# Kernel tuning notes

Hardware: AMD Instinct MI355X
Metric: run time of the kernel (lower is better)

## Reference

```python
import jax, jax.numpy as jnp
import numpy as np

B, S, D, H = 2, 2048, 1024, 16
HD = D // H  # head_dim = 64


def setup_inputs() -> dict:
    key = jax.random.key(0)
    ks = jax.random.split(key, 12)
    sc = 0.02
    return {
        "query": jax.random.normal(ks[0], (B, S, D), jnp.float32),
        "key": jax.random.normal(ks[1], (B, S, D), jnp.float32),
        "value": jax.random.normal(ks[2], (B, S, D), jnp.float32),
        "key_padding_mask": jax.random.randint(ks[3], (B, S), 0, 2).astype(bool),
        "attn_mask": jax.random.randint(ks[4], (B, S), 0, 2).astype(bool),
        "is_casual": 0,
        "Wq": jax.random.normal(ks[5], (D, D), jnp.float32) * sc,
        "bq": jnp.zeros((D,), jnp.float32),
        "Wk": jax.random.normal(ks[6], (D, D), jnp.float32) * sc,
        "bk": jnp.zeros((D,), jnp.float32),
        "Wv": jax.random.normal(ks[7], (D, D), jnp.float32) * sc,
        "bv": jnp.zeros((D,), jnp.float32),
        "Wo": jax.random.normal(ks[8], (D, D), jnp.float32) * sc,
        "bo": jnp.zeros((D,), jnp.float32),
    }


def reference(query, key, value, key_padding_mask, attn_mask, is_casual,
              Wq, bq, Wk, bk, Wv, bv, Wo, bo):
    b, s, _ = query.shape
    # projections (torch Linear: x @ W.T + b)
    Q = query @ Wq.T + bq
    K = key @ Wk.T + bk
    V = value @ Wv.T + bv
    # [B, H, S, HD]
    Q = Q.reshape(b, s, H, HD).transpose(0, 2, 1, 3)
    K = K.reshape(b, s, H, HD).transpose(0, 2, 1, 3)
    V = V.reshape(b, s, H, HD).transpose(0, 2, 1, 3)
    scores = jnp.einsum("bhqd,bhkd->bhqk", Q, K) / jnp.sqrt(jnp.float32(HD))
    neg_inf = jnp.float32(-jnp.inf)
    # both masks broadcast over the key axis: [B,1,1,S]
    scores = jnp.where(key_padding_mask[:, None, None, :], neg_inf, scores)
    scores = jnp.where(attn_mask[:, None, None, :], neg_inf, scores)
    # is_casual only applies in training mode; eval reference: no causal mask, no dropout
    attn = jax.nn.softmax(scores, axis=-1)
    x = jnp.einsum("bhqk,bhkd->bhqd", attn, V)
    x = x.transpose(0, 2, 1, 3).reshape(b, s, D)
    return x @ Wo.T + bo
```

## Files before the change

### kernel.cpp

```cpp
#include <hip/hip_runtime.h>


typedef __attribute__((ext_vector_type(8))) short short8;
typedef __attribute__((ext_vector_type(4))) float f32x4;
typedef __attribute__((ext_vector_type(4))) int int32x4;

#define MFMA16(a, b, c) __builtin_amdgcn_mfma_f32_16x16x32_bf16(a, b, c, 0, 0, 0)

#define GLL16(gp, lp) __builtin_amdgcn_global_load_lds( \
    (const __attribute__((address_space(1))) void*)(gp), \
    (__attribute__((address_space(3))) void*)(lp), 16, 0, 0)

static __device__ __forceinline__ unsigned short f2bf(float x) {
    unsigned int u = __float_as_uint(x);
    u = (u + 0x7fffu + ((u >> 16) & 1u)) >> 16;
    return (unsigned short)u;
}

__global__ __launch_bounds__(256)
void scan_kernel(const int* __restrict__ kpm, const int* __restrict__ am,
                 int* __restrict__ map, int* __restrict__ cnt)
{
    const int b = blockIdx.x, tid = threadIdx.x;
    const int lane = tid & 63, wave = tid >> 6;
    __shared__ int wtot[4];
    int flag[8]; int c = 0;
    const int base = b * 2048 + tid * 8;
#pragma unroll
    for (int e = 0; e < 8; ++e) {
        flag[e] = (kpm[base + e] | am[base + e]) ? 0 : 1;
        c += flag[e];
    }
    int pre = c;
#pragma unroll
    for (int off = 1; off < 64; off <<= 1) {
        const int t = __shfl_up(pre, off, 64);
        if (lane >= off) pre += t;
    }
    if (lane == 63) wtot[wave] = pre;
    __syncthreads();
    int woff = 0;
#pragma unroll
    for (int w = 0; w < 4; ++w) if (w < wave) woff += wtot[w];
    const int total = wtot[0] + wtot[1] + wtot[2] + wtot[3];
    if (tid == 0) cnt[b] = total;
    int off = b * 2048 + woff + (pre - c);
    const int s0 = tid * 8;
#pragma unroll
    for (int e = 0; e < 8; ++e)
        if (flag[e]) map[off++] = s0 + e;
    __syncthreads();
    const int first = (total > 0) ? map[b * 2048] : 0;
    for (int j = total + tid; j < 2048; j += 256)
        map[b * 2048 + j] = first;
}

__global__ __launch_bounds__(256)
void conv_many(const float* __restrict__ s0, unsigned short* __restrict__ d0, int n0,
               const float* __restrict__ s1, unsigned short* __restrict__ d1, int n1,
               const float* __restrict__ s2, unsigned short* __restrict__ d2, int n2,
               const float* __restrict__ s3, unsigned short* __restrict__ d3, int n3,
               const float* __restrict__ s4, unsigned short* __restrict__ d4, int n4,
               const float* __restrict__ s5, unsigned short* __restrict__ d5, int n5)
{
    const int y = blockIdx.y;
    const float* s; unsigned short* d; int n;
    if (y == 0)      { s = s0; d = d0; n = n0; }
    else if (y == 1) { s = s1; d = d1; n = n1; }
    else if (y == 2) { s = s2; d = d2; n = n2; }
    else if (y == 3) { s = s3; d = d3; n = n3; }
    else if (y == 4) { s = s4; d = d4; n = n4; }
    else             { s = s5; d = d5; n = n5; }
    const int i = (blockIdx.x * 256 + threadIdx.x) * 8;
    if (i >= n) return;
    const float4 a = *(const float4*)(s + i);
    const float4 b = *(const float4*)(s + i + 4);
    ushort4 lo, hi;
    lo.x = f2bf(a.x); lo.y = f2bf(a.y); lo.z = f2bf(a.z); lo.w = f2bf(a.w);
    hi.x = f2bf(b.x); hi.y = f2bf(b.y); hi.z = f2bf(b.z); hi.w = f2bf(b.w);
    *(ushort4*)(d + i) = lo;
    *(ushort4*)(d + i + 4) = hi;
}

template<int OUT_MODE, bool GATHER>
static __device__ __forceinline__
void gemm_core(int sub, const unsigned short* __restrict__ A, const unsigned short* __restrict__ Wb,
               const float* __restrict__ bias, float alpha, void* __restrict__ outp,
               unsigned short* sm, const int* __restrict__ map, const int* __restrict__ cnt)
{
    constexpr int N = 1024, K = 1024;
    const int xcd = sub & 7, loc = sub >> 3;
    const int m0 = (xcd * 4 + (loc >> 4)) * 128;
    const int n0 = (loc & 15) * 64;

    const int tid = threadIdx.x, lane = tid & 63, wave = tid >> 6;
    const int lr = lane & 15, quad = lane >> 4;
    const int wm = (wave >> 1) * 64, wn = (wave & 1) * 32;
    const int lr3 = lane >> 3;
    const int qcs = (lane & 7) ^ lr3;

    const int bb = m0 >> 11;
    int arow[4];
    if constexpr (GATHER) {
        const int cntb = cnt[bb];
        int cnt64 = (cntb + 63) & ~63;
        if (cnt64 < 64) cnt64 = 64;
        if ((m0 & 2047) >= cnt64) return;
#pragma unroll
        for (int n = 0; n < 4; n++) {
            const int row = (wave * 4 + n) * 8 + lr3;
            arow[n] = bb * 2048 + map[bb * 2048 + (m0 & 2047) + row];
        }
    } else {
#pragma unroll
        for (int n = 0; n < 4; n++)
            arow[n] = m0 + (wave * 4 + n) * 8 + lr3;
    }

    f32x4 acc[4][2];
#pragma unroll
    for (int mt = 0; mt < 4; mt++)
#pragma unroll
        for (int nt = 0; nt < 2; nt++) acc[mt][nt] = (f32x4){0.f, 0.f, 0.f, 0.f};

    auto stg = [&](int t) {
        unsigned short* Asb = sm + (t & 1) * 12288;
        unsigned short* Bsb = Asb + 8192;
        const int k0 = t * 64;
#pragma unroll
        for (int n = 0; n < 4; n++) {
            const int W = wave * 4 + n;
            GLL16(A + (size_t)arow[n] * K + k0 + qcs * 8, Asb + W * 512);
        }
#pragma unroll
        for (int n = 0; n < 2; n++) {
            const int W = wave * 2 + n;
            const int row = W * 8 + lr3;
            GLL16(Wb + (size_t)(n0 + row) * K + k0 + qcs * 8, Bsb + W * 512);
        }
    };

    stg(0);

    for (int it = 0; it < 16; ++it) {
        __syncthreads();
        if (it + 1 < 16) stg(it + 1);
        const unsigned short* Asc = sm + (it & 1) * 12288;
        const unsigned short* Bsc = Asc + 8192;
#pragma unroll
        for (int kc = 0; kc < 2; kc++) {
            short8 af[4], bfr[2];
#pragma unroll
            for (int mt = 0; mt < 4; mt++) {
                const int r = wm + mt * 16 + lr;
                af[mt] = *(const short8*)&Asc[(r * 8 + ((kc * 4 + quad) ^ (r & 7))) * 8];
            }
#pragma unroll
            for (int nt = 0; nt < 2; nt++) {
                const int r = wn + nt * 16 + lr;
                bfr[nt] = *(const short8*)&Bsc[(r * 8 + ((kc * 4 + quad) ^ (r & 7))) * 8];
            }
#pragma unroll
            for (int mt = 0; mt < 4; mt++)
#pragma unroll
                for (int nt = 0; nt < 2; nt++)
                    acc[mt][nt] = MFMA16(af[mt], bfr[nt], acc[mt][nt]);
        }
    }

    if constexpr (OUT_MODE == 2) {
        constexpr int LDT = 136;
        __syncthreads();
        unsigned short* Ts = sm;
#pragma unroll
        for (int mt = 0; mt < 4; mt++)
#pragma unroll
            for (int nt = 0; nt < 2; nt++) {
                const int dd = wn + nt * 16 + lr;
                const int ss = wm + mt * 16 + quad * 4;
                const int j = n0 + dd;
                ushort4 tv;
                tv.x = f2bf(alpha * (acc[mt][nt][0] + bias[j]));
                tv.y = f2bf(alpha * (acc[mt][nt][1] + bias[j]));
                tv.z = f2bf(alpha * (acc[mt][nt][2] + bias[j]));
                tv.w = f2bf(alpha * (acc[mt][nt][3] + bias[j]));
                *(ushort4*)&Ts[dd * LDT + ss] = tv;
            }
        __syncthreads();
        const int b = m0 >> 11, hh = (n0 >> 6) & 15, sbase = m0 & 2047;
        const int row = tid >> 2, c4 = (tid & 3) * 32;
        unsigned short* dst = (unsigned short*)outp
            + (((size_t)(b * 16 + hh) * 64) + row) * 2048 + sbase + c4;
#pragma unroll
        for (int t = 0; t < 4; ++t)
            *(short8*)&dst[t * 8] = *(const short8*)&Ts[row * LDT + c4 + t * 8];
        return;
    }

#pragma unroll
    for (int mt = 0; mt < 4; mt++)
#pragma unroll
        for (int nt = 0; nt < 2; nt++)
#pragma unroll
            for (int r = 0; r < 4; r++) {
                const int i = m0 + wm + mt * 16 + quad * 4 + r;
                const int j = n0 + wn + nt * 16 + lr;
                const float val = alpha * (acc[mt][nt][r] + bias[j]);
                if constexpr (OUT_MODE == 0) {
                    ((float*)outp)[(size_t)i * N + j] = val;
                } else {
                    const int b = i >> 11, s = i & 2047, hh = j >> 6, dd = j & 63;
                    ((unsigned short*)outp)[(((size_t)(b * 16 + hh) * 2048) + s) * 64 + dd] = f2bf(val);
                }
            }
}

__global__ __launch_bounds__(256)
void gemm_qv(const unsigned short* __restrict__ qb, const unsigned short* __restrict__ wqb,
             const float* __restrict__ bq, float alpha_q, void* __restrict__ Qh,
             const unsigned short* __restrict__ vb, const unsigned short* __restrict__ wvb,
             const float* __restrict__ bv, void* __restrict__ Vt,
             const int* __restrict__ map, const int* __restrict__ cnt)
{
    __shared__ unsigned short sm[24576];
    const int id = blockIdx.x, sub = id & 511;
    if (id < 512) gemm_core<1, false>(sub, qb, wqb, bq, alpha_q, Qh, sm, nullptr, nullptr);
    else          gemm_core<2, true >(sub, vb, wvb, bv, 1.0f,   Vt, sm, map, cnt);
}

template<int OUT_MODE, bool GATHER>
__global__ __launch_bounds__(256)
void gemm_one(const unsigned short* __restrict__ A, const unsigned short* __restrict__ Wb,
              const float* __restrict__ bias, float alpha, void* __restrict__ outp,
              const int* __restrict__ map, const int* __restrict__ cnt)
{
    __shared__ unsigned short sm[24576];
    gemm_core<OUT_MODE, GATHER>(blockIdx.x, A, Wb, bias, alpha, outp, sm, map, cnt);
}

__global__ __launch_bounds__(256)
void attn_kernel(const unsigned short* __restrict__ Qh, const unsigned short* __restrict__ Kh,
                 const unsigned short* __restrict__ Vt, const int* __restrict__ kpm,
                 const int* __restrict__ am, unsigned short* __restrict__ ctx)
{
    const int qb = blockIdx.x, bh = blockIdx.y, b = bh >> 4, h = bh & 15;
    const int q0 = qb * 64;
    const int tid = threadIdx.x, lane = tid & 63, wave = tid >> 6;
    const int lr = lane & 15, quad = lane >> 4;

    __shared__ unsigned short Ks[2][64 * 64];
    __shared__ unsigned short Vs[2][64 * 64];
    __shared__ int wred[4];

    {
        int c = 0;
        const int mb = b * 2048 + tid * 8;
#pragma unroll
        for (int e = 0; e < 8; ++e)
            c += (kpm[mb + e] | am[mb + e]) ? 0 : 1;
#pragma unroll
        for (int off = 32; off > 0; off >>= 1)
            c += __shfl_xor(c, off, 64);
        if (lane == 0) wred[wave] = c;
    }
    __syncthreads();
    const int cntb = wred[0] + wred[1] + wred[2] + wred[3];
    const int nits = (cntb > 0) ? ((cntb + 63) >> 6) : 1;

    const unsigned short* Kbh = Kh + (size_t)bh * 2048 * 64;
    const unsigned short* Vbh = Vt + (size_t)bh * 64 * 2048;

    const int lr3 = lane >> 3;
    const int qcs = (lane & 7) ^ lr3;

    auto stage = [&](int buf, int k0) {
#pragma unroll
        for (int n = 0; n < 2; ++n) {
            const int W = wave + n * 4;
            const int r = W * 8 + lr3;
            GLL16(Kbh + (size_t)(k0 + r) * 64 + qcs * 8, &Ks[buf][W * 512]);
            GLL16(Vbh + (size_t)r * 2048 + k0 + qcs * 8, &Vs[buf][W * 512]);
        }
    };

    const unsigned short* Qbase = Qh + ((size_t)bh * 2048 + q0 + wave * 16 + lr) * 64 + quad * 8;
    const short8 qf0 = *(const short8*)Qbase;
    const short8 qf1 = *(const short8*)(Qbase + 32);

    short8 onesA;
#pragma unroll
    for (int j = 0; j < 8; j++) onesA[j] = (short)0x3F80;

    f32x4 o[4];
    f32x4 lacc = (f32x4){0.f, 0.f, 0.f, 0.f};
#pragma unroll
    for (int nt = 0; nt < 4; nt++) o[nt] = (f32x4){0.f, 0.f, 0.f, 0.f};

    const int srcA = (quad & 1) * 32 + lr;
    const int srcB = srcA + 16;

    int koff[2][2][2], voff[2][4];
#pragma unroll
    for (int s32 = 0; s32 < 2; ++s32) {
#pragma unroll
        for (int tt = 0; tt < 2; ++tt) {
            const int kk = (s32 * 2 + tt) * 16 + lr;
            koff[s32][tt][0] = (kk * 8 + (quad ^ (kk & 7))) * 8;
            koff[s32][tt][1] = (kk * 8 + ((quad + 4) ^ (kk & 7))) * 8;
        }
#pragma unroll
        for (int nt = 0; nt < 4; ++nt) {
            const int d = nt * 16 + lr;
            const int qc = s32 * 4 + quad;
            voff[s32][nt] = (d * 8 + (qc ^ (d & 7))) * 8;
        }
    }

    auto tile = [&](const unsigned short* __restrict__ Kb,
                    const unsigned short* __restrict__ Vb, int k0) {
#pragma unroll
        for (int s32 = 0; s32 < 2; ++s32) {
            unsigned int pk[2][2];
#pragma unroll
            for (int tt = 0; tt < 2; ++tt) {
                const short8 kf0 = *(const short8*)&Kb[koff[s32][tt][0]];
                const short8 kf1 = *(const short8*)&Kb[koff[s32][tt][1]];
                f32x4 z;
                if (k0 + 64 <= cntb) {
                    z = (f32x4){0.f, 0.f, 0.f, 0.f};
                } else {
                    const int jb = k0 + (s32 * 2 + tt) * 16 + quad * 4;
#pragma unroll
                    for (int r = 0; r < 4; ++r)
                        z[r] = (jb + r < cntb) ? 0.f : -1e5f;
                }
                z = MFMA16(kf0, qf0, z);
                z = MFMA16(kf1, qf1, z);
                const float p0 = __builtin_amdgcn_exp2f(z[0]);
                const float p1 = __builtin_amdgcn_exp2f(z[1]);
                const float p2 = __builtin_amdgcn_exp2f(z[2]);
                const float p3 = __builtin_amdgcn_exp2f(z[3]);
                pk[tt][0] = ((unsigned)f2bf(p1) << 16) | f2bf(p0);
                pk[tt][1] = ((unsigned)f2bf(p3) << 16) | f2bf(p2);
            }
            const int a0 = __shfl((int)pk[0][0], srcA, 64);
            const int a1 = __shfl((int)pk[0][1], srcA, 64);
            const int a2 = __shfl((int)pk[0][0], srcB, 64);
            const int a3 = __shfl((int)pk[0][1], srcB, 64);
            const int c0 = __shfl((int)pk[1][0], srcA, 64);
            const int c1 = __shfl((int)pk[1][1], srcA, 64);
            const int c2 = __shfl((int)pk[1][0], srcB, 64);
            const int c3 = __shfl((int)pk[1][1], srcB, 64);
            const bool hi = quad >= 2;
            union { int32x4 i; short8 s; } u;
            u.i = (int32x4){hi ? c0 : a0, hi ? c1 : a1, hi ? c2 : a2, hi ? c3 : a3};
            const short8 pb = u.s;

            lacc = MFMA16(onesA, pb, lacc);
#pragma unroll
            for (int nt = 0; nt < 4; ++nt) {
                const short8 vf = *(const short8*)&Vb[voff[s32][nt]];
                o[nt] = MFMA16(vf, pb, o[nt]);
            }
        }
    };

    stage(0, 0);

    for (int it = 0; it < nits; ++it) {
        __syncthreads();
        if (it + 1 < nits) stage((it + 1) & 1, (it + 1) * 64);
        if (it & 1) tile(Ks[1], Vs[1], it * 64);
        else        tile(Ks[0], Vs[0], it * 64);
    }

    const float linv = 1.f / lacc[0];
    const int srow = q0 + wave * 16 + lr;
#pragma unroll
    for (int nt = 0; nt < 4; ++nt) {
        ushort4 pk4;
        pk4.x = f2bf(o[nt][0] * linv);
        pk4.y = f2bf(o[nt][1] * linv);
        pk4.z = f2bf(o[nt][2] * linv);
        pk4.w = f2bf(o[nt][3] * linv);
        *(ushort4*)&ctx[((size_t)(b * 2048 + srow)) * 1024 + h * 64 + nt * 16 + quad * 4] = pk4;
    }
}

extern "C" void kernel_launch(void* const* d_in, const int* in_sizes, int n_in,
                              void* d_out, int out_size, void* d_ws, size_t ws_size,
                              hipStream_t stream)
{
    const float* query = (const float*)d_in[0];
    const float* key_  = (const float*)d_in[1];
    const float* value = (const float*)d_in[2];
    const int* kpm     = (const int*)d_in[3];
    const int* am      = (const int*)d_in[4];
    const float* Wq = (const float*)d_in[6];
    const float* bq = (const float*)d_in[7];
    const float* Wk = (const float*)d_in[8];
    const float* bk = (const float*)d_in[9];
    const float* Wv = (const float*)d_in[10];
    const float* bv = (const float*)d_in[11];
    const float* Wo = (const float*)d_in[12];
    const float* bo = (const float*)d_in[13];

    unsigned short* ws16 = (unsigned short*)d_ws;
    unsigned short* Qh  = ws16;
    unsigned short* kbn = ws16 + (1u << 22);
    unsigned short* wob = ws16 + (1u << 22);
    unsigned short* Vt  = ws16 + (2u << 22);
    unsigned short* ctx = ws16 + 3 * (1u << 22);
    unsigned short* wqb = ctx;
    unsigned short* wvb = ctx + (1u << 20);
    unsigned short* wkb = ctx + (2u << 20);
    int* map = (int*)(ctx + (3u << 20));
    int* cnt = map + 4096;

    unsigned short* ob  = (unsigned short*)d_out;
    unsigned short* qb  = ob;
    unsigned short* vb  = ob + (1u << 22);
    unsigned short* Khd = ob;

    const dim3 blk(256);
    const float alpha_q = 0.125f * 1.4426950408889634f;

    scan_kernel<<<2, blk, 0, stream>>>(kpm, am, map, cnt);
    conv_many<<<dim3(2048, 6), blk, 0, stream>>>(
        query, qb,  1 << 22,
        value, vb,  1 << 22,
        key_,  kbn, 1 << 22,
        Wq,    wqb, 1 << 20,
        Wv,    wvb, 1 << 20,
        Wk,    wkb, 1 << 20);
    gemm_qv<<<1024, blk, 0, stream>>>(qb, wqb, bq, alpha_q, (void*)Qh, vb, wvb, bv, (void*)Vt,
                                      map, cnt);
    gemm_one<1, true><<<512, blk, 0, stream>>>(kbn, wkb, bk, 1.0f, (void*)Khd, map, cnt);
    conv_many<<<dim3(512, 1), blk, 0, stream>>>(
        Wo, wob, 1 << 20,
        nullptr, nullptr, 0, nullptr, nullptr, 0,
        nullptr, nullptr, 0, nullptr, nullptr, 0, nullptr, nullptr, 0);
    attn_kernel<<<dim3(32, 32), blk, 0, stream>>>(Qh, Khd, Vt, kpm, am, ctx);
    gemm_one<0, false><<<512, blk, 0, stream>>>(ctx, wob, bo, 1.0f, d_out, nullptr, nullptr);
}
```

Before: 207.1 us.

## Double query rows per attention block and fold mask scan into conversion launch

The attention kernel now has each block handle 128 query rows instead of 64. Each wave holds two sets of Q fragments and accumulators, so every K/V tile staged in LDS is used for twice as many queries and total K/V traffic is halved. This raises register pressure and halves the attention grid to 512 blocks, which may lower occupancy. The separate mask scan kernel is also merged into the input conversion launch as an extra grid row, and the Wo conversion uses a simpler dedicated kernel, removing one launch.

Result: no change. 207.4 us (+0.1%).

```diff
diff --git a/kernel.cpp b/kernel.cpp
--- a/kernel.cpp
+++ b/kernel.cpp
@@ -18,52 +18,52 @@
 }
 
 __global__ __launch_bounds__(256)
-void scan_kernel(const int* __restrict__ kpm, const int* __restrict__ am,
-                 int* __restrict__ map, int* __restrict__ cnt)
-{
-    const int b = blockIdx.x, tid = threadIdx.x;
-    const int lane = tid & 63, wave = tid >> 6;
-    __shared__ int wtot[4];
-    int flag[8]; int c = 0;
-    const int base = b * 2048 + tid * 8;
-#pragma unroll
-    for (int e = 0; e < 8; ++e) {
-        flag[e] = (kpm[base + e] | am[base + e]) ? 0 : 1;
-        c += flag[e];
-    }
-    int pre = c;
-#pragma unroll
-    for (int off = 1; off < 64; off <<= 1) {
-        const int t = __shfl_up(pre, off, 64);
-        if (lane >= off) pre += t;
-    }
-    if (lane == 63) wtot[wave] = pre;
-    __syncthreads();
-    int woff = 0;
-#pragma unroll
-    for (int w = 0; w < 4; ++w) if (w < wave) woff += wtot[w];
-    const int total = wtot[0] + wtot[1] + wtot[2] + wtot[3];
-    if (tid == 0) cnt[b] = total;
-    int off = b * 2048 + woff + (pre - c);
-    const int s0 = tid * 8;
-#pragma unroll
-    for (int e = 0; e < 8; ++e)
-        if (flag[e]) map[off++] = s0 + e;
-    __syncthreads();
-    const int first = (total > 0) ? map[b * 2048] : 0;
-    for (int j = total + tid; j < 2048; j += 256)
-        map[b * 2048 + j] = first;
-}
-
-__global__ __launch_bounds__(256)
-void conv_many(const float* __restrict__ s0, unsigned short* __restrict__ d0, int n0,
+void conv_scan(const float* __restrict__ s0, unsigned short* __restrict__ d0, int n0,
                const float* __restrict__ s1, unsigned short* __restrict__ d1, int n1,
                const float* __restrict__ s2, unsigned short* __restrict__ d2, int n2,
                const float* __restrict__ s3, unsigned short* __restrict__ d3, int n3,
                const float* __restrict__ s4, unsigned short* __restrict__ d4, int n4,
-               const float* __restrict__ s5, unsigned short* __restrict__ d5, int n5)
+               const float* __restrict__ s5, unsigned short* __restrict__ d5, int n5,
+               const int* __restrict__ kpm, const int* __restrict__ am,
+               int* __restrict__ map, int* __restrict__ cnt)
 {
     const int y = blockIdx.y;
+    if (y == 6) {
+        if (blockIdx.x >= 2) return;
+        const int b = blockIdx.x, tid = threadIdx.x;
+        const int lane = tid & 63, wave = tid >> 6;
+        __shared__ int wtot[4];
+        int flag[8]; int c = 0;
+        const int base = b * 2048 + tid * 8;
+#pragma unroll
+        for (int e = 0; e < 8; ++e) {
+            flag[e] = (kpm[base + e] | am[base + e]) ? 0 : 1;
+            c += flag[e];
+        }
+        int pre = c;
+#pragma unroll
+        for (int off = 1; off < 64; off <<= 1) {
+            const int t = __shfl_up(pre, off, 64);
+            if (lane >= off) pre += t;
+        }
+        if (lane == 63) wtot[wave] = pre;
+        __syncthreads();
+        int woff = 0;
+#pragma unroll
+        for (int w = 0; w < 4; ++w) if (w < wave) woff += wtot[w];
+        const int total = wtot[0] + wtot[1] + wtot[2] + wtot[3];
+        if (tid == 0) cnt[b] = total;
+        int off = b * 2048 + woff + (pre - c);
+        const int s0i = tid * 8;
+#pragma unroll
+        for (int e = 0; e < 8; ++e)
+            if (flag[e]) map[off++] = s0i + e;
+        __syncthreads();
+        const int first = (total > 0) ? map[b * 2048] : 0;
+        for (int j = total + tid; j < 2048; j += 256)
+            map[b * 2048 + j] = first;
+        return;
+    }
     const float* s; unsigned short* d; int n;
     if (y == 0)      { s = s0; d = d0; n = n0; }
     else if (y == 1) { s = s1; d = d1; n = n1; }
@@ -82,6 +82,20 @@
     *(ushort4*)(d + i + 4) = hi;
 }
 
+__global__ __launch_bounds__(256)
+void conv_one(const float* __restrict__ s, unsigned short* __restrict__ d, int n)
+{
+    const int i = (blockIdx.x * 256 + threadIdx.x) * 8;
+    if (i >= n) return;
+    const float4 a = *(const float4*)(s + i);
+    const float4 b = *(const float4*)(s + i + 4);
+    ushort4 lo, hi;
+    lo.x = f2bf(a.x); lo.y = f2bf(a.y); lo.z = f2bf(a.z); lo.w = f2bf(a.w);
+    hi.x = f2bf(b.x); hi.y = f2bf(b.y); hi.z = f2bf(b.z); hi.w = f2bf(b.w);
+    *(ushort4*)(d + i) = lo;
+    *(ushort4*)(d + i + 4) = hi;
+}
+
 template<int OUT_MODE, bool GATHER>
 static __device__ __forceinline__
 void gemm_core(int sub, const unsigned short* __restrict__ A, const unsigned short* __restrict__ Wb,
@@ -244,7 +258,7 @@
                  const int* __restrict__ am, unsigned short* __restrict__ ctx)
 {
     const int qb = blockIdx.x, bh = blockIdx.y, b = bh >> 4, h = bh & 15;
-    const int q0 = qb * 64;
+    const int q0 = qb * 128;
     const int tid = threadIdx.x, lane = tid & 63, wave = tid >> 6;
     const int lr = lane & 15, quad = lane >> 4;
 
@@ -284,17 +298,23 @@
     };
 
     const unsigned short* Qbase = Qh + ((size_t)bh * 2048 + q0 + wave * 16 + lr) * 64 + quad * 8;
-    const short8 qf0 = *(const short8*)Qbase;
-    const short8 qf1 = *(const short8*)(Qbase + 32);
+    const short8 qf0a = *(const short8*)Qbase;
+    const short8 qf1a = *(const short8*)(Qbase + 32);
+    const short8 qf0b = *(const short8*)(Qbase + 64 * 64);
+    const short8 qf1b = *(const short8*)(Qbase + 64 * 64 + 32);
 
     short8 onesA;
 #pragma unroll
     for (int j = 0; j < 8; j++) onesA[j] = (short)0x3F80;
 
-    f32x4 o[4];
-    f32x4 lacc = (f32x4){0.f, 0.f, 0.f, 0.f};
-#pragma unroll
-    for (int nt = 0; nt < 4; nt++) o[nt] = (f32x4){0.f, 0.f, 0.f, 0.f};
+    f32x4 oA[4], oB[4];
+    f32x4 laccA = (f32x4){0.f, 0.f, 0.f, 0.f};
+    f32x4 laccB = (f32x4){0.f, 0.f, 0.f, 0.f};
+#pragma unroll
+    for (int nt = 0; nt < 4; nt++) {
+        oA[nt] = (f32x4){0.f, 0.f, 0.f, 0.f};
+        oB[nt] = (f32x4){0.f, 0.f, 0.f, 0.f};
+    }
 
     const int srcA = (quad & 1) * 32 + lr;
     const int srcB = srcA + 16;
@@ -320,47 +340,70 @@
                     const unsigned short* __restrict__ Vb, int k0) {
 #pragma unroll
         for (int s32 = 0; s32 < 2; ++s32) {
-            unsigned int pk[2][2];
+            unsigned int pkA[2][2], pkB[2][2];
 #pragma unroll
             for (int tt = 0; tt < 2; ++tt) {
                 const short8 kf0 = *(const short8*)&Kb[koff[s32][tt][0]];
                 const short8 kf1 = *(const short8*)&Kb[koff[s32][tt][1]];
-                f32x4 z;
+                f32x4 zm;
                 if (k0 + 64 <= cntb) {
-                    z = (f32x4){0.f, 0.f, 0.f, 0.f};
+                    zm = (f32x4){0.f, 0.f, 0.f, 0.f};
                 } else {
                     const int jb = k0 + (s32 * 2 + tt) * 16 + quad * 4;
 #pragma unroll
                     for (int r = 0; r < 4; ++r)
-                        z[r] = (jb + r < cntb) ? 0.f : -1e5f;
+                        zm[r] = (jb + r < cntb) ? 0.f : -1e5f;
                 }
-                z = MFMA16(kf0, qf0, z);
-                z = MFMA16(kf1, qf1, z);
-                const float p0 = __builtin_amdgcn_exp2f(z[0]);
-                const float p1 = __builtin_amdgcn_exp2f(z[1]);
-                const float p2 = __builtin_amdgcn_exp2f(z[2]);
-                const float p3 = __builtin_amdgcn_exp2f(z[3]);
-                pk[tt][0] = ((unsigned)f2bf(p1) << 16) | f2bf(p0);
-                pk[tt][1] = ((unsigned)f2bf(p3) << 16) | f2bf(p2);
-            }
-            const int a0 = __shfl((int)pk[0][0], srcA, 64);
-            const int a1 = __shfl((int)pk[0][1], srcA, 64);
-            const int a2 = __shfl((int)pk[0][0], srcB, 64);
-            const int a3 = __shfl((int)pk[0][1], srcB, 64);
-            const int c0 = __shfl((int)pk[1][0], srcA, 64);
-            const int c1 = __shfl((int)pk[1][1], srcA, 64);
-            const int c2 = __shfl((int)pk[1][0], srcB, 64);
-            const int c3 = __shfl((int)pk[1][1], srcB, 64);
+                f32x4 zA = zm, zB = zm;
+                zA = MFMA16(kf0, qf0a, zA);
+                zA = MFMA16(kf1, qf1a, zA);
+                zB = MFMA16(kf0, qf0b, zB);
+                zB = MFMA16(kf1, qf1b, zB);
+                pkA[tt][0] = ((unsigned)f2bf(__builtin_amdgcn_exp2f(zA[1])) << 16)
+                           | f2bf(__builtin_amdgcn_exp2f(zA[0]));
+                pkA[tt][1] = ((unsigned)f2bf(__builtin_amdgcn_exp2f(zA[3])) << 16)
+                           | f2bf(__builtin_amdgcn_exp2f(zA[2]));
+                pkB[tt][0] = ((unsigned)f2bf(__builtin_amdgcn_exp2f(zB[1])) << 16)
+                           | f2bf(__builtin_amdgcn_exp2f(zB[0]));
+                pkB[tt][1] = ((unsigned)f2bf(__builtin_amdgcn_exp2f(zB[3])) << 16)
+                           | f2bf(__builtin_amdgcn_exp2f(zB[2]));
+            }
             const bool hi = quad >= 2;
-            union { int32x4 i; short8 s; } u;
-            u.i = (int32x4){hi ? c0 : a0, hi ? c1 : a1, hi ? c2 : a2, hi ? c3 : a3};
-            const short8 pb = u.s;
-
-            lacc = MFMA16(onesA, pb, lacc);
+            short8 pbA, pbB;
+            {
+                const int a0 = __shfl((int)pkA[0][0], srcA, 64);
+                const int a1 = __shfl((int)pkA[0][1], srcA, 64);
+                const int a2 = __shfl((int)pkA[0][0], srcB, 64);
+                const int a3 = __shfl((int)pkA[0][1], srcB, 64);
+                const int c0 = __shfl((int)pkA[1][0], srcA, 64);
+                const int c1 = __shfl((int)pkA[1][1], srcA, 64);
+                const int c2 = __shfl((int)pkA[1][0], srcB, 64);
+                const int c3 = __shfl((int)pkA[1][1], srcB, 64);
+                union { int32x4 i; short8 s; } u;
+                u.i = (int32x4){hi ? c0 : a0, hi ? c1 : a1, hi ? c2 : a2, hi ? c3 : a3};
+                pbA = u.s;
+            }
+            {
+                const int a0 = __shfl((int)pkB[0][0], srcA, 64);
+                const int a1 = __shfl((int)pkB[0][1], srcA, 64);
+                const int a2 = __shfl((int)pkB[0][0], srcB, 64);
+                const int a3 = __shfl((int)pkB[0][1], srcB, 64);
+                const int c0 = __shfl((int)pkB[1][0], srcA, 64);
+                const int c1 = __shfl((int)pkB[1][1], srcA, 64);
+                const int c2 = __shfl((int)pkB[1][0], srcB, 64);
+                const int c3 = __shfl((int)pkB[1][1], srcB, 64);
+                union { int32x4 i; short8 s; } u;
+                u.i = (int32x4){hi ? c0 : a0, hi ? c1 : a1, hi ? c2 : a2, hi ? c3 : a3};
+                pbB = u.s;
+            }
+
+            laccA = MFMA16(onesA, pbA, laccA);
+            laccB = MFMA16(onesA, pbB, laccB);
 #pragma unroll
             for (int nt = 0; nt < 4; ++nt) {
                 const short8 vf = *(const short8*)&Vb[voff[s32][nt]];
-                o[nt] = MFMA16(vf, pb, o[nt]);
+                oA[nt] = MFMA16(vf, pbA, oA[nt]);
+                oB[nt] = MFMA16(vf, pbB, oB[nt]);
             }
         }
     };
@@ -374,16 +417,23 @@
         else        tile(Ks[0], Vs[0], it * 64);
     }
 
-    const float linv = 1.f / lacc[0];
-    const int srow = q0 + wave * 16 + lr;
+    const float linvA = 1.f / laccA[0];
+    const float linvB = 1.f / laccB[0];
+    const int srowA = q0 + wave * 16 + lr;
+    const int srowB = srowA + 64;
 #pragma unroll
     for (int nt = 0; nt < 4; ++nt) {
-        ushort4 pk4;
-        pk4.x = f2bf(o[nt][0] * linv);
-        pk4.y = f2bf(o[nt][1] * linv);
-        pk4.z = f2bf(o[nt][2] * linv);
-        pk4.w = f2bf(o[nt][3] * linv);
-        *(ushort4*)&ctx[((size_t)(b * 2048 + srow)) * 1024 + h * 64 + nt * 16 + quad * 4] = pk4;
+        ushort4 p4;
+        p4.x = f2bf(oA[nt][0] * linvA);
+        p4.y = f2bf(oA[nt][1] * linvA);
+        p4.z = f2bf(oA[nt][2] * linvA);
+        p4.w = f2bf(oA[nt][3] * linvA);
+        *(ushort4*)&ctx[((size_t)(b * 2048 + srowA)) * 1024 + h * 64 + nt * 16 + quad * 4] = p4;
+        p4.x = f2bf(oB[nt][0] * linvB);
+        p4.y = f2bf(oB[nt][1] * linvB);
+        p4.z = f2bf(oB[nt][2] * linvB);
+        p4.w = f2bf(oB[nt][3] * linvB);
+        *(ushort4*)&ctx[((size_t)(b * 2048 + srowB)) * 1024 + h * 64 + nt * 16 + quad * 4] = p4;
     }
 }
 
@@ -425,21 +475,18 @@
     const dim3 blk(256);
     const float alpha_q = 0.125f * 1.4426950408889634f;
 
-    scan_kernel<<<2, blk, 0, stream>>>(kpm, am, map, cnt);
-    conv_many<<<dim3(2048, 6), blk, 0, stream>>>(
+    conv_scan<<<dim3(2048, 7), blk, 0, stream>>>(
         query, qb,  1 << 22,
         value, vb,  1 << 22,
         key_,  kbn, 1 << 22,
         Wq,    wqb, 1 << 20,
         Wv,    wvb, 1 << 20,
-        Wk,    wkb, 1 << 20);
+        Wk,    wkb, 1 << 20,
+        kpm, am, map, cnt);
     gemm_qv<<<1024, blk, 0, stream>>>(qb, wqb, bq, alpha_q, (void*)Qh, vb, wvb, bv, (void*)Vt,
                                       map, cnt);
     gemm_one<1, true><<<512, blk, 0, stream>>>(kbn, wkb, bk, 1.0f, (void*)Khd, map, cnt);
-    conv_many<<<dim3(512, 1), blk, 0, stream>>>(
-        Wo, wob, 1 << 20,
-        nullptr, nullptr, 0, nullptr, nullptr, 0,
-        nullptr, nullptr, 0, nullptr, nullptr, 0, nullptr, nullptr, 0);
-    attn_kernel<<<dim3(32, 32), blk, 0, stream>>>(Qh, Khd, Vt, kpm, am, ctx);
+    conv_one<<<dim3(512), blk, 0, stream>>>(Wo, wob, 1 << 20);
+    attn_kernel<<<dim3(16, 32), blk, 0, stream>>>(Qh, Khd, Vt, kpm, am, ctx);
     gemm_one<0, false><<<512, blk, 0, stream>>>(ctx, wob, bo, 1.0f, d_out, nullptr, nullptr);
 }
```

## Fuse mask scan into conversion kernel and read K/V directly from global in attention

Applied to the files above, without the earlier changes.

The mask-scan kernel is merged into the fp32-to-bf16 conversion launch as an extra grid row, which removes one kernel launch. A dedicated single-buffer conversion kernel replaces the generic one for Wo. The attention kernel drops its double-buffered LDS staging of K and V via global_load_lds and instead loads MFMA fragments straight from global memory, relying on L1/L2 caching. This removes the barriers and LDS traffic, but each wave now re-reads K/V tiles from global with less coalesced, uncached-in-LDS accesses, which risks higher memory latency in the hot loop.

After: 246.0 us. 1.19x slower.

```diff
diff --git a/kernel.cpp b/kernel.cpp
--- a/kernel.cpp
+++ b/kernel.cpp
@@ -18,52 +18,52 @@
 }
 
 __global__ __launch_bounds__(256)
-void scan_kernel(const int* __restrict__ kpm, const int* __restrict__ am,
-                 int* __restrict__ map, int* __restrict__ cnt)
-{
-    const int b = blockIdx.x, tid = threadIdx.x;
-    const int lane = tid & 63, wave = tid >> 6;
-    __shared__ int wtot[4];
-    int flag[8]; int c = 0;
-    const int base = b * 2048 + tid * 8;
-#pragma unroll
-    for (int e = 0; e < 8; ++e) {
-        flag[e] = (kpm[base + e] | am[base + e]) ? 0 : 1;
-        c += flag[e];
-    }
-    int pre = c;
-#pragma unroll
-    for (int off = 1; off < 64; off <<= 1) {
-        const int t = __shfl_up(pre, off, 64);
-        if (lane >= off) pre += t;
-    }
-    if (lane == 63) wtot[wave] = pre;
-    __syncthreads();
-    int woff = 0;
-#pragma unroll
-    for (int w = 0; w < 4; ++w) if (w < wave) woff += wtot[w];
-    const int total = wtot[0] + wtot[1] + wtot[2] + wtot[3];
-    if (tid == 0) cnt[b] = total;
-    int off = b * 2048 + woff + (pre - c);
-    const int s0 = tid * 8;
-#pragma unroll
-    for (int e = 0; e < 8; ++e)
-        if (flag[e]) map[off++] = s0 + e;
-    __syncthreads();
-    const int first = (total > 0) ? map[b * 2048] : 0;
-    for (int j = total + tid; j < 2048; j += 256)
-        map[b * 2048 + j] = first;
-}
-
-__global__ __launch_bounds__(256)
-void conv_many(const float* __restrict__ s0, unsigned short* __restrict__ d0, int n0,
+void conv_scan(const float* __restrict__ s0, unsigned short* __restrict__ d0, int n0,
                const float* __restrict__ s1, unsigned short* __restrict__ d1, int n1,
                const float* __restrict__ s2, unsigned short* __restrict__ d2, int n2,
                const float* __restrict__ s3, unsigned short* __restrict__ d3, int n3,
                const float* __restrict__ s4, unsigned short* __restrict__ d4, int n4,
-               const float* __restrict__ s5, unsigned short* __restrict__ d5, int n5)
+               const float* __restrict__ s5, unsigned short* __restrict__ d5, int n5,
+               const int* __restrict__ kpm, const int* __restrict__ am,
+               int* __restrict__ map, int* __restrict__ cnt)
 {
     const int y = blockIdx.y;
+    if (y == 6) {
+        if (blockIdx.x >= 2) return;
+        const int b = blockIdx.x, tid = threadIdx.x;
+        const int lane = tid & 63, wave = tid >> 6;
+        __shared__ int wtot[4];
+        int flag[8]; int c = 0;
+        const int base = b * 2048 + tid * 8;
+#pragma unroll
+        for (int e = 0; e < 8; ++e) {
+            flag[e] = (kpm[base + e] | am[base + e]) ? 0 : 1;
+            c += flag[e];
+        }
+        int pre = c;
+#pragma unroll
+        for (int off = 1; off < 64; off <<= 1) {
+            const int t = __shfl_up(pre, off, 64);
+            if (lane >= off) pre += t;
+        }
+        if (lane == 63) wtot[wave] = pre;
+        __syncthreads();
+        int woff = 0;
+#pragma unroll
+        for (int w = 0; w < 4; ++w) if (w < wave) woff += wtot[w];
+        const int total = wtot[0] + wtot[1] + wtot[2] + wtot[3];
+        if (tid == 0) cnt[b] = total;
+        int off = b * 2048 + woff + (pre - c);
+        const int s0i = tid * 8;
+#pragma unroll
+        for (int e = 0; e < 8; ++e)
+            if (flag[e]) map[off++] = s0i + e;
+        __syncthreads();
+        const int first = (total > 0) ? map[b * 2048] : 0;
+        for (int j = total + tid; j < 2048; j += 256)
+            map[b * 2048 + j] = first;
+        return;
+    }
     const float* s; unsigned short* d; int n;
     if (y == 0)      { s = s0; d = d0; n = n0; }
     else if (y == 1) { s = s1; d = d1; n = n1; }
@@ -82,6 +82,20 @@
     *(ushort4*)(d + i + 4) = hi;
 }
 
+__global__ __launch_bounds__(256)
+void conv_one(const float* __restrict__ s, unsigned short* __restrict__ d, int n)
+{
+    const int i = (blockIdx.x * 256 + threadIdx.x) * 8;
+    if (i >= n) return;
+    const float4 a = *(const float4*)(s + i);
+    const float4 b = *(const float4*)(s + i + 4);
+    ushort4 lo, hi;
+    lo.x = f2bf(a.x); lo.y = f2bf(a.y); lo.z = f2bf(a.z); lo.w = f2bf(a.w);
+    hi.x = f2bf(b.x); hi.y = f2bf(b.y); hi.z = f2bf(b.z); hi.w = f2bf(b.w);
+    *(ushort4*)(d + i) = lo;
+    *(ushort4*)(d + i + 4) = hi;
+}
+
 template<int OUT_MODE, bool GATHER>
 static __device__ __forceinline__
 void gemm_core(int sub, const unsigned short* __restrict__ A, const unsigned short* __restrict__ Wb,
@@ -248,8 +262,6 @@
     const int tid = threadIdx.x, lane = tid & 63, wave = tid >> 6;
     const int lr = lane & 15, quad = lane >> 4;
 
-    __shared__ unsigned short Ks[2][64 * 64];
-    __shared__ unsigned short Vs[2][64 * 64];
     __shared__ int wred[4];
 
     {
@@ -270,19 +282,6 @@
     const unsigned short* Kbh = Kh + (size_t)bh * 2048 * 64;
     const unsigned short* Vbh = Vt + (size_t)bh * 64 * 2048;
 
-    const int lr3 = lane >> 3;
-    const int qcs = (lane & 7) ^ lr3;
-
-    auto stage = [&](int buf, int k0) {
-#pragma unroll
-        for (int n = 0; n < 2; ++n) {
-            const int W = wave + n * 4;
-            const int r = W * 8 + lr3;
-            GLL16(Kbh + (size_t)(k0 + r) * 64 + qcs * 8, &Ks[buf][W * 512]);
-            GLL16(Vbh + (size_t)r * 2048 + k0 + qcs * 8, &Vs[buf][W * 512]);
-        }
-    };
-
     const unsigned short* Qbase = Qh + ((size_t)bh * 2048 + q0 + wave * 16 + lr) * 64 + quad * 8;
     const short8 qf0 = *(const short8*)Qbase;
     const short8 qf1 = *(const short8*)(Qbase + 32);
@@ -299,32 +298,16 @@
     const int srcA = (quad & 1) * 32 + lr;
     const int srcB = srcA + 16;
 
-    int koff[2][2][2], voff[2][4];
-#pragma unroll
-    for (int s32 = 0; s32 < 2; ++s32) {
-#pragma unroll
-        for (int tt = 0; tt < 2; ++tt) {
-            const int kk = (s32 * 2 + tt) * 16 + lr;
-            koff[s32][tt][0] = (kk * 8 + (quad ^ (kk & 7))) * 8;
-            koff[s32][tt][1] = (kk * 8 + ((quad + 4) ^ (kk & 7))) * 8;
-        }
-#pragma unroll
-        for (int nt = 0; nt < 4; ++nt) {
-            const int d = nt * 16 + lr;
-            const int qc = s32 * 4 + quad;
-            voff[s32][nt] = (d * 8 + (qc ^ (d & 7))) * 8;
-        }
-    }
-
-    auto tile = [&](const unsigned short* __restrict__ Kb,
-                    const unsigned short* __restrict__ Vb, int k0) {
+    for (int it = 0; it < nits; ++it) {
+        const int k0 = it * 64;
 #pragma unroll
         for (int s32 = 0; s32 < 2; ++s32) {
             unsigned int pk[2][2];
 #pragma unroll
             for (int tt = 0; tt < 2; ++tt) {
-                const short8 kf0 = *(const short8*)&Kb[koff[s32][tt][0]];
-                const short8 kf1 = *(const short8*)&Kb[koff[s32][tt][1]];
+                const int kk = k0 + (s32 * 2 + tt) * 16 + lr;
+                const short8 kf0 = *(const short8*)&Kbh[(size_t)kk * 64 + quad * 8];
+                const short8 kf1 = *(const short8*)&Kbh[(size_t)kk * 64 + quad * 8 + 32];
                 f32x4 z;
                 if (k0 + 64 <= cntb) {
                     z = (f32x4){0.f, 0.f, 0.f, 0.f};
@@ -359,19 +342,11 @@
             lacc = MFMA16(onesA, pb, lacc);
 #pragma unroll
             for (int nt = 0; nt < 4; ++nt) {
-                const short8 vf = *(const short8*)&Vb[voff[s32][nt]];
+                const int d = nt * 16 + lr;
+                const short8 vf = *(const short8*)&Vbh[(size_t)d * 2048 + k0 + (s32 * 4 + quad) * 8];
                 o[nt] = MFMA16(vf, pb, o[nt]);
             }
         }
-    };
-
-    stage(0, 0);
-
-    for (int it = 0; it < nits; ++it) {
-        __syncthreads();
-        if (it + 1 < nits) stage((it + 1) & 1, (it + 1) * 64);
-        if (it & 1) tile(Ks[1], Vs[1], it * 64);
-        else        tile(Ks[0], Vs[0], it * 64);
     }
 
     const float linv = 1.f / lacc[0];
@@ -425,21 +400,18 @@
     const dim3 blk(256);
     const float alpha_q = 0.125f * 1.4426950408889634f;
 
-    scan_kernel<<<2, blk, 0, stream>>>(kpm, am, map, cnt);
-    conv_many<<<dim3(2048, 6), blk, 0, stream>>>(
+    conv_scan<<<dim3(2048, 7), blk, 0, stream>>>(
         query, qb,  1 << 22,
         value, vb,  1 << 22,
         key_,  kbn, 1 << 22,
         Wq,    wqb, 1 << 20,
         Wv,    wvb, 1 << 20,
-        Wk,    wkb, 1 << 20);
+        Wk,    wkb, 1 << 20,
+        kpm, am, map, cnt);
     gemm_qv<<<1024, blk, 0, stream>>>(qb, wqb, bq, alpha_q, (void*)Qh, vb, wvb, bv, (void*)Vt,
                                       map, cnt);
     gemm_one<1, true><<<512, blk, 0, stream>>>(kbn, wkb, bk, 1.0f, (void*)Khd, map, cnt);
-    conv_many<<<dim3(512, 1), blk, 0, stream>>>(
-        Wo, wob, 1 << 20,
-        nullptr, nullptr, 0, nullptr, nullptr, 0,
-        nullptr, nullptr, 0, nullptr, nullptr, 0, nullptr, nullptr, 0);
+    conv_one<<<dim3(512), blk, 0, stream>>>(Wo, wob, 1 << 20);
     attn_kernel<<<dim3(32, 32), blk, 0, stream>>>(Qh, Khd, Vt, kpm, am, ctx);
     gemm_one<0, false><<<512, blk, 0, stream>>>(ctx, wob, bo, 1.0f, d_out, nullptr, nullptr);
 }
```
